# Kernel optimization log

Hardware: AMD Instinct MI355X
Metric: run time of the kernel (lower is better)

The kernel has to match this reference:

```python
import jax, jax.numpy as jnp
import numpy as np
import math

D_MODEL = 1024
N_HEADS = 16


def setup_inputs() -> dict:
    key = jax.random.key(0)
    ks = jax.random.split(key, 11)
    N, L, S = 2, 2048, 2048
    d = D_MODEL
    s = 1.0 / math.sqrt(d)
    return {
        "queries": jax.random.normal(ks[0], (N, L, d), dtype=jnp.float32),
        "keys": jax.random.normal(ks[1], (N, S, d), dtype=jnp.float32),
        "values": jax.random.normal(ks[2], (N, S, d), dtype=jnp.float32),
        # torch nn.Linear weights are [out_features, in_features]
        "Wq": jax.random.normal(ks[3], (d, d), dtype=jnp.float32) * s,
        "bq": jax.random.normal(ks[4], (d,), dtype=jnp.float32) * s,
        "Wk": jax.random.normal(ks[5], (d, d), dtype=jnp.float32) * s,
        "bk": jax.random.normal(ks[6], (d,), dtype=jnp.float32) * s,
        "Wv": jax.random.normal(ks[7], (d, d), dtype=jnp.float32) * s,
        "bv": jax.random.normal(ks[8], (d,), dtype=jnp.float32) * s,
        "Wo": jax.random.normal(ks[9], (d, d), dtype=jnp.float32) * s,
        "bo": jax.random.normal(ks[10], (d,), dtype=jnp.float32) * s,
    }


def reference(queries, keys, values, Wq, bq, Wk, bk, Wv, bv, Wo, bo):
    N, L, _ = queries.shape
    S = keys.shape[1]
    H = N_HEADS
    # projections (torch Linear: x @ W.T + b), reshape to heads
    q = (queries @ Wq.T + bq).reshape(N, L, H, -1)
    k = (keys @ Wk.T + bk).reshape(N, S, H, -1)
    v = (values @ Wv.T + bv).reshape(N, S, H, -1)
    D = k.shape[-1]
    # full attention score map [N, L, H, S]
    sm = jnp.einsum('nlhd,nshd->nlhs', q, k) / math.sqrt(D)
    # causal mask: position l attends to s <= l
    causal_mask = jnp.triu(jnp.ones((L, S), dtype=bool), k=1)  # True = masked
    sm = jnp.where(causal_mask[None, :, None, :], -jnp.inf, sm)
    sm = jax.nn.softmax(sm, axis=-1)
    attn = jnp.einsum('nlhs,nshd->nlhd', sm, v)  # [N, L, H, D]
    new_values = attn.reshape(N, L, H * D)
    return new_values @ Wo.T + bo
```

## Files before the change

kernel.cpp:

```cpp
#include <hip/hip_runtime.h>

typedef unsigned short u16;
typedef unsigned int u32;
typedef __attribute__((ext_vector_type(8))) short bf16x8;
typedef __attribute__((ext_vector_type(4))) float f32x4;
typedef __attribute__((ext_vector_type(16))) float f32x16;
typedef __attribute__((ext_vector_type(4))) float floatx4;
typedef __attribute__((ext_vector_type(4))) u16 u16x4;

__device__ __forceinline__ u16 f2bf(float x) {
  union { float f; u32 u; } c; c.f = x;
  return (u16)((c.u + 0x7fffu + ((c.u >> 16) & 1u)) >> 16);
}
__device__ __forceinline__ u32 packbf(float a, float b) {
  return (u32)f2bf(a) | ((u32)f2bf(b) << 16);
}
__device__ __forceinline__ u32 cvtpk(float lo, float hi) {
  u32 r;
  asm("v_cvt_pk_bf16_f32 %0, %1, %2" : "=v"(r) : "v"(lo), "v"(hi));
  return r;
}
__device__ __forceinline__ float bf2f(u16 v) {
  union { u32 u; float f; } c; c.u = (u32)v << 16; return c.f;
}

__device__ __forceinline__ void gload16(const u16* g, u16* l) {
  auto gp = (const __attribute__((address_space(1))) unsigned int*)g;
  auto lp = (__attribute__((address_space(3))) unsigned int*)l;
  __builtin_amdgcn_global_load_lds(gp, lp, 16, 0, 0);
}

__global__ void cvt7(const float* s0, const float* s1, const float* s2,
                     const float* s3, const float* s4, const float* s5, const float* s6,
                     u16* d0, u16* d1, u16* d2, u16* d3, u16* d4, u16* d5, u16* d6) {
  const int y = blockIdx.y;
  const float* s = (y == 0) ? s0 : (y == 1) ? s1 : (y == 2) ? s2 : (y == 3) ? s3
                  : (y == 4) ? s4 : (y == 5) ? s5 : s6;
  u16* d = (y == 0) ? d0 : (y == 1) ? d1 : (y == 2) ? d2 : (y == 3) ? d3
          : (y == 4) ? d4 : (y == 5) ? d5 : d6;
  const int n4 = (y < 3) ? (1 << 20) : (1 << 18);
  int i = blockIdx.x * 256 + threadIdx.x;
  if (i < n4) {
    floatx4 v = ((const floatx4*)s)[i];
    u16x4 o;
    o.x = f2bf(v.x); o.y = f2bf(v.y); o.z = f2bf(v.z); o.w = f2bf(v.w);
    ((u16x4*)d)[i] = o;
  }
}

__global__ __launch_bounds__(256) void gemm3(const u16* A0, const u16* A1, const u16* A2,
                                             const u16* W0, const u16* W1, const u16* W2,
                                             const float* b0, const float* b1, const float* b2,
                                             u16* o0, u16* o1, u16* o2) {
  __shared__ u16 lA[128 * 32];
  __shared__ u16 lB[128 * 32];
  const int z = blockIdx.z;
  const u16* A  = (z == 0) ? A0 : (z == 1) ? A1 : A2;
  const u16* Bw = (z == 0) ? W0 : (z == 1) ? W1 : W2;
  const float* bias = (z == 0) ? b0 : (z == 1) ? b1 : b2;
  u16* outp = (z == 0) ? o0 : (z == 1) ? o1 : o2;
  const float scl = (z == 0) ? (0.125f * 1.44269504089f) : 1.0f;

  const int tid = threadIdx.x;
  const int brow = blockIdx.y * 128, bcol = blockIdx.x * 128;
  const int lane = tid & 63, w = tid >> 6;
  const int wr = w >> 1, wc = w & 1;
  const int fr = lane & 15, fq = lane >> 4;
  f32x4 acc[4][4] = {};

  for (int k0 = 0; k0 < 1024; k0 += 32) {
    __syncthreads();
#pragma unroll
    for (int it = 0; it < 2; ++it) {
      int chunk = tid + it * 256;
      int row = chunk >> 2;
      int col = (chunk & 3) * 8;
      gload16(A  + (size_t)(brow + row) * 1024 + k0 + col, &lA[chunk * 8]);
      gload16(Bw + (size_t)(bcol + row) * 1024 + k0 + col, &lB[chunk * 8]);
    }
    __syncthreads();
    bf16x8 af[4], bfr[4];
#pragma unroll
    for (int m = 0; m < 4; ++m) af[m]  = *(const bf16x8*)&lA[(wr * 64 + m * 16 + fr) * 32 + fq * 8];
#pragma unroll
    for (int n = 0; n < 4; ++n) bfr[n] = *(const bf16x8*)&lB[(wc * 64 + n * 16 + fr) * 32 + fq * 8];
#pragma unroll
    for (int m = 0; m < 4; ++m)
#pragma unroll
      for (int n = 0; n < 4; ++n)
        acc[m][n] = __builtin_amdgcn_mfma_f32_16x16x32_bf16(af[m], bfr[n], acc[m][n], 0, 0, 0);
  }

#pragma unroll
  for (int m = 0; m < 4; ++m) {
#pragma unroll
    for (int n = 0; n < 4; ++n) {
      int colg = bcol + wc * 64 + n * 16 + fr;
      float bv = bias[colg];
#pragma unroll
      for (int j = 0; j < 4; ++j) {
        int rowg = brow + wr * 64 + m * 16 + fq * 4 + j;
        float v = (acc[m][n][j] + bv) * scl;
        int nb = rowg >> 11, l = rowg & 2047;
        int h = colg >> 6, dd = colg & 63;
        size_t idx = (z < 2) ? (((size_t)(nb * 16 + h) * 2048 + l) * 64 + dd)
                             : (((size_t)(nb * 16 + h) * 64 + dd) * 2048 + l);
        outp[idx] = f2bf(v);
      }
    }
  }
}

__global__ __launch_bounds__(256) void gemm_o(const u16* __restrict__ A,
                                              const u16* __restrict__ Bw,
                                              const float* __restrict__ bias,
                                              float* __restrict__ outp) {
  __shared__ u16 lA[128 * 32];
  __shared__ u16 lB[128 * 32];
  const int tid = threadIdx.x;
  const int brow = blockIdx.y * 128, bcol = blockIdx.x * 128;
  const int lane = tid & 63, w = tid >> 6;
  const int wr = w >> 1, wc = w & 1;
  const int fr = lane & 15, fq = lane >> 4;
  f32x4 acc[4][4] = {};

  for (int k0 = 0; k0 < 1024; k0 += 32) {
    __syncthreads();
#pragma unroll
    for (int it = 0; it < 2; ++it) {
      int chunk = tid + it * 256;
      int row = chunk >> 2;
      int col = (chunk & 3) * 8;
      gload16(A  + (size_t)(brow + row) * 1024 + k0 + col, &lA[chunk * 8]);
      gload16(Bw + (size_t)(bcol + row) * 1024 + k0 + col, &lB[chunk * 8]);
    }
    __syncthreads();
    bf16x8 af[4], bfr[4];
#pragma unroll
    for (int m = 0; m < 4; ++m) af[m]  = *(const bf16x8*)&lA[(wr * 64 + m * 16 + fr) * 32 + fq * 8];
#pragma unroll
    for (int n = 0; n < 4; ++n) bfr[n] = *(const bf16x8*)&lB[(wc * 64 + n * 16 + fr) * 32 + fq * 8];
#pragma unroll
    for (int m = 0; m < 4; ++m)
#pragma unroll
      for (int n = 0; n < 4; ++n)
        acc[m][n] = __builtin_amdgcn_mfma_f32_16x16x32_bf16(af[m], bfr[n], acc[m][n], 0, 0, 0);
  }

#pragma unroll
  for (int m = 0; m < 4; ++m) {
#pragma unroll
    for (int n = 0; n < 4; ++n) {
      int colg = bcol + wc * 64 + n * 16 + fr;
      float bv = bias[colg];
#pragma unroll
      for (int j = 0; j < 4; ++j) {
        int rowg = brow + wr * 64 + m * 16 + fq * 4 + j;
        outp[(size_t)rowg * 1024 + colg] = acc[m][n][j] + bv;
      }
    }
  }
}

__global__ __launch_bounds__(256) void attn_part(const u16* __restrict__ Qp,
                                                 const u16* __restrict__ Kp,
                                                 const u16* __restrict__ Vt,
                                                 u16* __restrict__ accP,
                                                 float* __restrict__ mP,
                                                 float* __restrict__ lP) {
  __shared__ u16 lK[2][2048];
  __shared__ u16 lV[2][2048];
  const int tid = threadIdx.x;
  const int lane = tid & 63, w = tid >> 6;
  const int bid = blockIdx.x;
  const int nh = bid / 40;
  const int j = bid - nh * 40;
  int p, t;
  if (j < 16)      { p = 0; t = j; }
  else if (j < 28) { p = 1; t = 4 + (j - 16); }
  else if (j < 36) { p = 2; t = 8 + (j - 28); }
  else             { p = 3; t = 12 + (j - 36); }
  const int i0 = p * 16;
  const int i1 = min(i0 + 16, (t + 1) * 4);
  const int col = lane & 31, hi = lane >> 5;
  const u16* Q = Qp + (size_t)nh * 2048 * 64;
  const u16* K = Kp + (size_t)nh * 2048 * 64;
  const u16* V = Vt + (size_t)nh * 64 * 2048;
  const int q = t * 128 + w * 32 + col;
  const int swz = (col & 7) << 4;

  const int kr  = tid >> 3;
  const int kin = ((tid & 7) * 16) ^ ((kr & 7) << 4);
  const int vd  = kr + ((kin >> 6) << 5);
  const int vs  = (kin & 63) >> 1;

  bf16x8 qf[4];
#pragma unroll
  for (int ks = 0; ks < 4; ++ks) qf[ks] = *(const bf16x8*)&Q[(size_t)q * 64 + ks * 16 + hi * 8];

  f32x16 acc0 = {}, acc1 = {};
  float mrow = -1e30f, lrow = 0.f;

  {
    const int s0 = i0 * 32;
    gload16(K + (size_t)(s0 + kr) * 64 + (kin >> 1), &lK[0][tid * 8]);
    gload16(V + (size_t)vd * 2048 + (s0 + vs),       &lV[0][tid * 8]);
  }
  __syncthreads();

  int cur = 0;
  for (int i = i0; i < i1; ++i) {
    if (i + 1 < i1) {
      const int s0n = (i + 1) * 32;
      gload16(K + (size_t)(s0n + kr) * 64 + (kin >> 1), &lK[cur ^ 1][tid * 8]);
      gload16(V + (size_t)vd * 2048 + (s0n + vs),       &lV[cur ^ 1][tid * 8]);
    }
    const int s0 = i * 32;
    f32x16 sc = {};
    __builtin_amdgcn_s_setprio(1);
#pragma unroll
    for (int ks = 0; ks < 4; ++ks) {
      bf16x8 kf = *(const bf16x8*)&lK[cur][col * 64 + (((ks * 32 + hi * 16) ^ swz) >> 1)];
      sc = __builtin_amdgcn_mfma_f32_32x32x16_bf16(kf, qf[ks], sc, 0, 0, 0);
    }
    __builtin_amdgcn_s_setprio(0);
    float pr[16];
    float pmax = -1e30f;
#pragma unroll
    for (int r = 0; r < 16; ++r) {
      int sr = (r & 3) + 8 * (r >> 2) + 4 * hi;
      float v = (s0 + sr > q) ? -1e30f : sc[r];
      pr[r] = v;
      pmax = fmaxf(pmax, v);
    }
    pmax = fmaxf(pmax, __shfl_xor(pmax, 32));
    if (!__all(pmax <= mrow + 8.f)) {
      float mnew = fmaxf(mrow, pmax);
      float alpha = exp2f(mrow - mnew);
#pragma unroll
      for (int r = 0; r < 16; ++r) { acc0[r] *= alpha; acc1[r] *= alpha; }
      lrow *= alpha;
      mrow = mnew;
    }
    float ps = 0.f;
#pragma unroll
    for (int r = 0; r < 16; ++r) { float pv = exp2f(pr[r] - mrow); pr[r] = pv; ps += pv; }
    ps += __shfl_xor(ps, 32);
    lrow += ps;

#pragma unroll
    for (int ks = 0; ks < 2; ++ks) {
      u32 A0 = cvtpk(pr[8 * ks + 0], pr[8 * ks + 1]);
      u32 A1 = cvtpk(pr[8 * ks + 2], pr[8 * ks + 3]);
      u32 B0 = cvtpk(pr[8 * ks + 4], pr[8 * ks + 5]);
      u32 B1 = cvtpk(pr[8 * ks + 6], pr[8 * ks + 7]);
      u32 t0 = __shfl_xor(hi ? A0 : B0, 32);
      u32 t1 = __shfl_xor(hi ? A1 : B1, 32);
      union { u32 u[4]; bf16x8 v; } pf;
      pf.u[0] = hi ? t0 : A0;
      pf.u[1] = hi ? t1 : A1;
      pf.u[2] = hi ? B0 : t0;
      pf.u[3] = hi ? B1 : t1;
      bf16x8 vf0 = *(const bf16x8*)&lV[cur][col * 64 + (((ks * 32 + hi * 16) ^ swz) >> 1)];
      bf16x8 vf1 = *(const bf16x8*)&lV[cur][col * 64 + (((64 + ks * 32 + hi * 16) ^ swz) >> 1)];
      __builtin_amdgcn_s_setprio(1);
      acc0 = __builtin_amdgcn_mfma_f32_32x32x16_bf16(vf0, pf.v, acc0, 0, 0, 0);
      acc1 = __builtin_amdgcn_mfma_f32_32x32x16_bf16(vf1, pf.v, acc1, 0, 0, 0);
      __builtin_amdgcn_s_setprio(0);
    }
    __syncthreads();
    cur ^= 1;
  }

  const int ql = w * 32 + col;
  u16* base = accP + (size_t)bid * 8192 + ql * 64;
#pragma unroll
  for (int rp = 0; rp < 8; ++rp) {
    int r = rp * 2;
    int d = (r & 3) + 8 * (r >> 2) + 4 * hi;
    *(u32*)&base[d]      = packbf(acc0[r], acc0[r + 1]);
    *(u32*)&base[32 + d] = packbf(acc1[r], acc1[r + 1]);
  }
  if (hi == 0) {
    mP[bid * 128 + ql] = mrow;
    lP[bid * 128 + ql] = lrow;
  }
}

__global__ void combineN(const u16* __restrict__ accP, const float* __restrict__ mP,
                         const float* __restrict__ lP, u16* __restrict__ at) {
  const int t = blockIdx.x >> 2;
  const int seg = blockIdx.x & 3;
  const int nh = blockIdx.y;
  const int ql = seg * 32 + (threadIdx.x >> 3);
  const int d0 = (threadIdx.x & 7) * 8;
  const int np = (t >> 2) + 1;
  const int s0 = nh * 40 + t;
  const int s1 = nh * 40 + 16 + (t - 4);
  const int s2 = nh * 40 + 28 + (t - 8);
  const int s3 = nh * 40 + 36 + (t - 12);

  float m = mP[s0 * 128 + ql];
  if (np > 1) m = fmaxf(m, mP[s1 * 128 + ql]);
  if (np > 2) m = fmaxf(m, mP[s2 * 128 + ql]);
  if (np > 3) m = fmaxf(m, mP[s3 * 128 + ql]);
  float w0 = exp2f(mP[s0 * 128 + ql] - m);
  float w1 = (np > 1) ? exp2f(mP[s1 * 128 + ql] - m) : 0.f;
  float w2 = (np > 2) ? exp2f(mP[s2 * 128 + ql] - m) : 0.f;
  float w3 = (np > 3) ? exp2f(mP[s3 * 128 + ql] - m) : 0.f;
  float l = lP[s0 * 128 + ql] * w0;
  if (np > 1) l += lP[s1 * 128 + ql] * w1;
  if (np > 2) l += lP[s2 * 128 + ql] * w2;
  if (np > 3) l += lP[s3 * 128 + ql] * w3;
  const float inv = 1.f / l;
  w0 *= inv; w1 *= inv; w2 *= inv; w3 *= inv;

  float o[8] = {};
  {
    const bf16x8 a = *(const bf16x8*)&accP[(size_t)s0 * 8192 + ql * 64 + d0];
#pragma unroll
    for (int k = 0; k < 8; ++k) o[k] += bf2f((u16)a[k]) * w0;
  }
  if (np > 1) {
    const bf16x8 a = *(const bf16x8*)&accP[(size_t)s1 * 8192 + ql * 64 + d0];
#pragma unroll
    for (int k = 0; k < 8; ++k) o[k] += bf2f((u16)a[k]) * w1;
  }
  if (np > 2) {
    const bf16x8 a = *(const bf16x8*)&accP[(size_t)s2 * 8192 + ql * 64 + d0];
#pragma unroll
    for (int k = 0; k < 8; ++k) o[k] += bf2f((u16)a[k]) * w2;
  }
  if (np > 3) {
    const bf16x8 a = *(const bf16x8*)&accP[(size_t)s3 * 8192 + ql * 64 + d0];
#pragma unroll
    for (int k = 0; k < 8; ++k) o[k] += bf2f((u16)a[k]) * w3;
  }

  const int nb = nh >> 4, h = nh & 15;
  u16* op = &at[((size_t)(nb * 2048 + t * 128 + ql)) * 1024 + h * 64 + d0];
#pragma unroll
  for (int jj = 0; jj < 4; ++jj)
    *(u32*)&op[2 * jj] = packbf(o[2 * jj], o[2 * jj + 1]);
}

extern "C" void kernel_launch(void* const* d_in, const int* in_sizes, int n_in,
                              void* d_out, int out_size, void* d_ws, size_t ws_size,
                              hipStream_t stream) {
  const float* queries = (const float*)d_in[0];
  const float* keys    = (const float*)d_in[1];
  const float* values  = (const float*)d_in[2];
  const float* Wq = (const float*)d_in[3]; const float* bq = (const float*)d_in[4];
  const float* Wk = (const float*)d_in[5]; const float* bk = (const float*)d_in[6];
  const float* Wv = (const float*)d_in[7]; const float* bv = (const float*)d_in[8];
  const float* Wo = (const float*)d_in[9]; const float* bo = (const float*)d_in[10];
  float* out = (float*)d_out;
  char* ws = (char*)d_ws;

  const size_t MB = 1u << 20;
  u16* xq  = (u16*)(ws + 0 * MB);
  u16* xk  = (u16*)(ws + 8 * MB);
  u16* xv  = (u16*)(ws + 16 * MB);
  u16* wqb = (u16*)(ws + 24 * MB);
  u16* wkb = (u16*)(ws + 26 * MB);
  u16* wvb = (u16*)(ws + 28 * MB);
  u16* wob = (u16*)(ws + 30 * MB);
  u16* qp  = (u16*)(ws + 32 * MB);
  u16* kp  = (u16*)(ws + 40 * MB);
  u16* vt  = (u16*)(ws + 48 * MB);
  u16* at  = xq;
  u16*   accP = (u16*)(ws + 8 * MB);
  float* mPp  = (float*)(ws + 28 * MB);
  float* lPp  = (float*)(ws + 28 * MB + 1280 * 128 * sizeof(float));

  cvt7<<<dim3(4096, 7), 256, 0, stream>>>(queries, keys, values, Wq, Wk, Wv, Wo,
                                          xq, xk, xv, wqb, wkb, wvb, wob);
  gemm3<<<dim3(8, 32, 3), 256, 0, stream>>>(xq, xk, xv, wqb, wkb, wvb,
                                            bq, bk, bv, qp, kp, vt);
  attn_part<<<1280, 256, 0, stream>>>(qp, kp, vt, accP, mPp, lPp);
  combineN<<<dim3(64, 32), 256, 0, stream>>>(accP, mPp, lPp, at);
  gemm_o<<<dim3(8, 32), 256, 0, stream>>>(at, wob, bo, out);
}
```

Measured before the change: 249.7 us.

## Double-buffer GEMM tiles, widen attention KV tiles, skip masked sub-tiles, remap blocks

```diff
diff --git a/kernel.cpp b/kernel.cpp
--- a/kernel.cpp
+++ b/kernel.cpp
@@ -29,6 +29,10 @@
   auto lp = (__attribute__((address_space(3))) unsigned int*)l;
   __builtin_amdgcn_global_load_lds(gp, lp, 16, 0, 0);
 }
+
+#define WAIT_VM4() asm volatile("s_waitcnt vmcnt(4)" ::: "memory")
+#define WAIT_VM0() asm volatile("s_waitcnt vmcnt(0)" ::: "memory")
+#define WAIT_LGKM0() asm volatile("s_waitcnt lgkmcnt(0)" ::: "memory")
 
 __global__ void cvt7(const float* s0, const float* s1, const float* s2,
                      const float* s3, const float* s4, const float* s5, const float* s6,
@@ -52,8 +56,8 @@
                                              const u16* W0, const u16* W1, const u16* W2,
                                              const float* b0, const float* b1, const float* b2,
                                              u16* o0, u16* o1, u16* o2) {
-  __shared__ u16 lA[128 * 32];
-  __shared__ u16 lB[128 * 32];
+  __shared__ u16 lA[2][128 * 32];
+  __shared__ u16 lB[2][128 * 32];
   const int z = blockIdx.z;
   const u16* A  = (z == 0) ? A0 : (z == 1) ? A1 : A2;
   const u16* Bw = (z == 0) ? W0 : (z == 1) ? W1 : W2;
@@ -68,27 +72,47 @@
   const int fr = lane & 15, fq = lane >> 4;
   f32x4 acc[4][4] = {};
 
-  for (int k0 = 0; k0 < 1024; k0 += 32) {
-    __syncthreads();
+  auto stageg = [&](int ks, int bb) {
 #pragma unroll
     for (int it = 0; it < 2; ++it) {
       int chunk = tid + it * 256;
       int row = chunk >> 2;
-      int col = (chunk & 3) * 8;
-      gload16(A  + (size_t)(brow + row) * 1024 + k0 + col, &lA[chunk * 8]);
-      gload16(Bw + (size_t)(bcol + row) * 1024 + k0 + col, &lB[chunk * 8]);
-    }
-    __syncthreads();
+      int colb = (chunk & 3) * 8;
+      gload16(A  + (size_t)(brow + row) * 1024 + ks * 32 + colb, &lA[bb][chunk * 8]);
+      gload16(Bw + (size_t)(bcol + row) * 1024 + ks * 32 + colb, &lB[bb][chunk * 8]);
+    }
+  };
+
+  float bvr[4];
+#pragma unroll
+  for (int n = 0; n < 4; ++n) bvr[n] = bias[bcol + wc * 64 + n * 16 + fr];
+
+  stageg(0, 0);
+  WAIT_VM0();
+  __builtin_amdgcn_s_barrier();
+
+  for (int kk = 0; kk < 32; ++kk) {
+    const int cur = kk & 1;
+    if (kk + 1 < 32) { stageg(kk + 1, cur ^ 1); WAIT_VM4(); }
+    else             { WAIT_VM0(); }
+    __builtin_amdgcn_s_barrier();
+    __builtin_amdgcn_sched_barrier(0);
+
     bf16x8 af[4], bfr[4];
 #pragma unroll
-    for (int m = 0; m < 4; ++m) af[m]  = *(const bf16x8*)&lA[(wr * 64 + m * 16 + fr) * 32 + fq * 8];
-#pragma unroll
-    for (int n = 0; n < 4; ++n) bfr[n] = *(const bf16x8*)&lB[(wc * 64 + n * 16 + fr) * 32 + fq * 8];
+    for (int m = 0; m < 4; ++m) af[m]  = *(const bf16x8*)&lA[cur][(wr * 64 + m * 16 + fr) * 32 + fq * 8];
+#pragma unroll
+    for (int n = 0; n < 4; ++n) bfr[n] = *(const bf16x8*)&lB[cur][(wc * 64 + n * 16 + fr) * 32 + fq * 8];
+    __builtin_amdgcn_s_setprio(1);
 #pragma unroll
     for (int m = 0; m < 4; ++m)
 #pragma unroll
       for (int n = 0; n < 4; ++n)
         acc[m][n] = __builtin_amdgcn_mfma_f32_16x16x32_bf16(af[m], bfr[n], acc[m][n], 0, 0, 0);
+    __builtin_amdgcn_s_setprio(0);
+
+    WAIT_LGKM0();
+    __builtin_amdgcn_s_barrier();
   }
 
 #pragma unroll
@@ -96,11 +120,10 @@
 #pragma unroll
     for (int n = 0; n < 4; ++n) {
       int colg = bcol + wc * 64 + n * 16 + fr;
-      float bv = bias[colg];
 #pragma unroll
       for (int j = 0; j < 4; ++j) {
         int rowg = brow + wr * 64 + m * 16 + fq * 4 + j;
-        float v = (acc[m][n][j] + bv) * scl;
+        float v = (acc[m][n][j] + bvr[n]) * scl;
         int nb = rowg >> 11, l = rowg & 2047;
         int h = colg >> 6, dd = colg & 63;
         size_t idx = (z < 2) ? (((size_t)(nb * 16 + h) * 2048 + l) * 64 + dd)
@@ -115,8 +138,8 @@
                                               const u16* __restrict__ Bw,
                                               const float* __restrict__ bias,
                                               float* __restrict__ outp) {
-  __shared__ u16 lA[128 * 32];
-  __shared__ u16 lB[128 * 32];
+  __shared__ u16 lA[2][128 * 32];
+  __shared__ u16 lB[2][128 * 32];
   const int tid = threadIdx.x;
   const int brow = blockIdx.y * 128, bcol = blockIdx.x * 128;
   const int lane = tid & 63, w = tid >> 6;
@@ -124,27 +147,47 @@
   const int fr = lane & 15, fq = lane >> 4;
   f32x4 acc[4][4] = {};
 
-  for (int k0 = 0; k0 < 1024; k0 += 32) {
-    __syncthreads();
+  auto stageg = [&](int ks, int bb) {
 #pragma unroll
     for (int it = 0; it < 2; ++it) {
       int chunk = tid + it * 256;
       int row = chunk >> 2;
-      int col = (chunk & 3) * 8;
-      gload16(A  + (size_t)(brow + row) * 1024 + k0 + col, &lA[chunk * 8]);
-      gload16(Bw + (size_t)(bcol + row) * 1024 + k0 + col, &lB[chunk * 8]);
-    }
-    __syncthreads();
+      int colb = (chunk & 3) * 8;
+      gload16(A  + (size_t)(brow + row) * 1024 + ks * 32 + colb, &lA[bb][chunk * 8]);
+      gload16(Bw + (size_t)(bcol + row) * 1024 + ks * 32 + colb, &lB[bb][chunk * 8]);
+    }
+  };
+
+  float bvr[4];
+#pragma unroll
+  for (int n = 0; n < 4; ++n) bvr[n] = bias[bcol + wc * 64 + n * 16 + fr];
+
+  stageg(0, 0);
+  WAIT_VM0();
+  __builtin_amdgcn_s_barrier();
+
+  for (int kk = 0; kk < 32; ++kk) {
+    const int cur = kk & 1;
+    if (kk + 1 < 32) { stageg(kk + 1, cur ^ 1); WAIT_VM4(); }
+    else             { WAIT_VM0(); }
+    __builtin_amdgcn_s_barrier();
+    __builtin_amdgcn_sched_barrier(0);
+
     bf16x8 af[4], bfr[4];
 #pragma unroll
-    for (int m = 0; m < 4; ++m) af[m]  = *(const bf16x8*)&lA[(wr * 64 + m * 16 + fr) * 32 + fq * 8];
-#pragma unroll
-    for (int n = 0; n < 4; ++n) bfr[n] = *(const bf16x8*)&lB[(wc * 64 + n * 16 + fr) * 32 + fq * 8];
+    for (int m = 0; m < 4; ++m) af[m]  = *(const bf16x8*)&lA[cur][(wr * 64 + m * 16 + fr) * 32 + fq * 8];
+#pragma unroll
+    for (int n = 0; n < 4; ++n) bfr[n] = *(const bf16x8*)&lB[cur][(wc * 64 + n * 16 + fr) * 32 + fq * 8];
+    __builtin_amdgcn_s_setprio(1);
 #pragma unroll
     for (int m = 0; m < 4; ++m)
 #pragma unroll
       for (int n = 0; n < 4; ++n)
         acc[m][n] = __builtin_amdgcn_mfma_f32_16x16x32_bf16(af[m], bfr[n], acc[m][n], 0, 0, 0);
+    __builtin_amdgcn_s_setprio(0);
+
+    WAIT_LGKM0();
+    __builtin_amdgcn_s_barrier();
   }
 
 #pragma unroll
@@ -152,11 +195,10 @@
 #pragma unroll
     for (int n = 0; n < 4; ++n) {
       int colg = bcol + wc * 64 + n * 16 + fr;
-      float bv = bias[colg];
 #pragma unroll
       for (int j = 0; j < 4; ++j) {
         int rowg = brow + wr * 64 + m * 16 + fq * 4 + j;
-        outp[(size_t)rowg * 1024 + colg] = acc[m][n][j] + bv;
+        outp[(size_t)rowg * 1024 + colg] = acc[m][n][j] + bvr[n];
       }
     }
   }
@@ -168,112 +210,132 @@
                                                  u16* __restrict__ accP,
                                                  float* __restrict__ mP,
                                                  float* __restrict__ lP) {
-  __shared__ u16 lK[2][2048];
-  __shared__ u16 lV[2][2048];
+  __shared__ u16 lK[2][4096];
+  __shared__ u16 lV[2][4096];
   const int tid = threadIdx.x;
   const int lane = tid & 63, w = tid >> 6;
-  const int bid = blockIdx.x;
-  const int nh = bid / 40;
-  const int j = bid - nh * 40;
+  const int bid = (int)blockIdx.x;
+  const int vbid = (bid & 7) * 160 + (bid >> 3);
+  const int nh = vbid / 40;
+  const int j = vbid - nh * 40;
   int p, t;
   if (j < 16)      { p = 0; t = j; }
   else if (j < 28) { p = 1; t = 4 + (j - 16); }
   else if (j < 36) { p = 2; t = 8 + (j - 28); }
   else             { p = 3; t = 12 + (j - 36); }
-  const int i0 = p * 16;
-  const int i1 = min(i0 + 16, (t + 1) * 4);
+  const int P0 = p * 8;
+  const int P1 = min(P0 + 8, 2 * (t + 1));
   const int col = lane & 31, hi = lane >> 5;
   const u16* Q = Qp + (size_t)nh * 2048 * 64;
   const u16* K = Kp + (size_t)nh * 2048 * 64;
   const u16* V = Vt + (size_t)nh * 64 * 2048;
-  const int q = t * 128 + w * 32 + col;
+  const int qbase = t * 128 + w * 32;
+  const int q = qbase + col;
   const int swz = (col & 7) << 4;
 
-  const int kr  = tid >> 3;
-  const int kin = ((tid & 7) * 16) ^ ((kr & 7) << 4);
-  const int vd  = kr + ((kin >> 6) << 5);
-  const int vs  = (kin & 63) >> 1;
+  auto stage = [&](int pp, int bb) {
+#pragma unroll
+    for (int it = 0; it < 2; ++it) {
+      int c = tid + it * 256;
+      int kr = c >> 3;
+      int kin = ((c & 7) * 16) ^ ((kr & 7) << 4);
+      gload16(K + (size_t)(pp * 64 + kr) * 64 + (kin >> 1), &lK[bb][c * 8]);
+      int tt = c >> 8, cc = c & 255;
+      int lr = cc >> 3;
+      int vin = ((cc & 7) * 16) ^ ((lr & 7) << 4);
+      int vd = lr + ((vin >> 6) << 5);
+      gload16(V + (size_t)vd * 2048 + pp * 64 + tt * 32 + ((vin & 63) >> 1),
+              &lV[bb][c * 8]);
+    }
+  };
 
   bf16x8 qf[4];
 #pragma unroll
   for (int ks = 0; ks < 4; ++ks) qf[ks] = *(const bf16x8*)&Q[(size_t)q * 64 + ks * 16 + hi * 8];
 
   f32x16 acc0 = {}, acc1 = {};
-  float mrow = -1e30f, lrow = 0.f;
-
-  {
-    const int s0 = i0 * 32;
-    gload16(K + (size_t)(s0 + kr) * 64 + (kin >> 1), &lK[0][tid * 8]);
-    gload16(V + (size_t)vd * 2048 + (s0 + vs),       &lV[0][tid * 8]);
-  }
-  __syncthreads();
-
-  int cur = 0;
-  for (int i = i0; i < i1; ++i) {
-    if (i + 1 < i1) {
-      const int s0n = (i + 1) * 32;
-      gload16(K + (size_t)(s0n + kr) * 64 + (kin >> 1), &lK[cur ^ 1][tid * 8]);
-      gload16(V + (size_t)vd * 2048 + (s0n + vs),       &lV[cur ^ 1][tid * 8]);
-    }
-    const int s0 = i * 32;
-    f32x16 sc = {};
-    __builtin_amdgcn_s_setprio(1);
-#pragma unroll
-    for (int ks = 0; ks < 4; ++ks) {
-      bf16x8 kf = *(const bf16x8*)&lK[cur][col * 64 + (((ks * 32 + hi * 16) ^ swz) >> 1)];
-      sc = __builtin_amdgcn_mfma_f32_32x32x16_bf16(kf, qf[ks], sc, 0, 0, 0);
-    }
-    __builtin_amdgcn_s_setprio(0);
-    float pr[16];
-    float pmax = -1e30f;
-#pragma unroll
-    for (int r = 0; r < 16; ++r) {
-      int sr = (r & 3) + 8 * (r >> 2) + 4 * hi;
-      float v = (s0 + sr > q) ? -1e30f : sc[r];
-      pr[r] = v;
-      pmax = fmaxf(pmax, v);
-    }
-    pmax = fmaxf(pmax, __shfl_xor(pmax, 32));
-    if (!__all(pmax <= mrow + 8.f)) {
-      float mnew = fmaxf(mrow, pmax);
-      float alpha = exp2f(mrow - mnew);
-#pragma unroll
-      for (int r = 0; r < 16; ++r) { acc0[r] *= alpha; acc1[r] *= alpha; }
-      lrow *= alpha;
-      mrow = mnew;
-    }
-    float ps = 0.f;
-#pragma unroll
-    for (int r = 0; r < 16; ++r) { float pv = exp2f(pr[r] - mrow); pr[r] = pv; ps += pv; }
-    ps += __shfl_xor(ps, 32);
-    lrow += ps;
-
-#pragma unroll
-    for (int ks = 0; ks < 2; ++ks) {
-      u32 A0 = cvtpk(pr[8 * ks + 0], pr[8 * ks + 1]);
-      u32 A1 = cvtpk(pr[8 * ks + 2], pr[8 * ks + 3]);
-      u32 B0 = cvtpk(pr[8 * ks + 4], pr[8 * ks + 5]);
-      u32 B1 = cvtpk(pr[8 * ks + 6], pr[8 * ks + 7]);
-      u32 t0 = __shfl_xor(hi ? A0 : B0, 32);
-      u32 t1 = __shfl_xor(hi ? A1 : B1, 32);
-      union { u32 u[4]; bf16x8 v; } pf;
-      pf.u[0] = hi ? t0 : A0;
-      pf.u[1] = hi ? t1 : A1;
-      pf.u[2] = hi ? B0 : t0;
-      pf.u[3] = hi ? B1 : t1;
-      bf16x8 vf0 = *(const bf16x8*)&lV[cur][col * 64 + (((ks * 32 + hi * 16) ^ swz) >> 1)];
-      bf16x8 vf1 = *(const bf16x8*)&lV[cur][col * 64 + (((64 + ks * 32 + hi * 16) ^ swz) >> 1)];
+  float mrow = -1e30f, lsum = 0.f;
+
+  stage(P0, 0);
+  WAIT_VM0();
+  __builtin_amdgcn_s_barrier();
+
+  for (int pp = P0; pp < P1; ++pp) {
+    const int buf = (pp - P0) & 1;
+    if (pp + 1 < P1) { stage(pp + 1, buf ^ 1); WAIT_VM4(); }
+    else             { WAIT_VM0(); }
+    __builtin_amdgcn_s_barrier();
+    __builtin_amdgcn_sched_barrier(0);
+
+#pragma unroll
+    for (int tt = 0; tt < 2; ++tt) {
+      const int s0 = pp * 64 + tt * 32;
+      if (s0 > qbase) continue;
+      f32x16 sc = {};
       __builtin_amdgcn_s_setprio(1);
-      acc0 = __builtin_amdgcn_mfma_f32_32x32x16_bf16(vf0, pf.v, acc0, 0, 0, 0);
-      acc1 = __builtin_amdgcn_mfma_f32_32x32x16_bf16(vf1, pf.v, acc1, 0, 0, 0);
+#pragma unroll
+      for (int ks = 0; ks < 4; ++ks) {
+        bf16x8 kf = *(const bf16x8*)&lK[buf][(tt * 32 + col) * 64 + (((ks * 32 + hi * 16) ^ swz) >> 1)];
+        sc = __builtin_amdgcn_mfma_f32_32x32x16_bf16(kf, qf[ks], sc, 0, 0, 0);
+      }
       __builtin_amdgcn_s_setprio(0);
-    }
-    __syncthreads();
-    cur ^= 1;
+      float pr[16];
+      float pmax = -1e30f;
+      if (s0 == qbase) {
+#pragma unroll
+        for (int r = 0; r < 16; ++r) {
+          int sr = (r & 3) + 8 * (r >> 2) + 4 * hi;
+          float v = (sr > col) ? -1e30f : sc[r];
+          pr[r] = v;
+          pmax = fmaxf(pmax, v);
+        }
+      } else {
+#pragma unroll
+        for (int r = 0; r < 16; ++r) { pr[r] = sc[r]; pmax = fmaxf(pmax, sc[r]); }
+      }
+      pmax = fmaxf(pmax, __shfl_xor(pmax, 32));
+      if (!__all(pmax <= mrow + 8.f)) {
+        float mnew = fmaxf(mrow, pmax);
+        float alpha = exp2f(mrow - mnew);
+#pragma unroll
+        for (int r = 0; r < 16; ++r) { acc0[r] *= alpha; acc1[r] *= alpha; }
+        lsum *= alpha;
+        mrow = mnew;
+      }
+      float ps = 0.f;
+#pragma unroll
+      for (int r = 0; r < 16; ++r) { float pv = exp2f(pr[r] - mrow); pr[r] = pv; ps += pv; }
+      ps += __shfl_xor(ps, 32);
+      lsum += ps;
+
+#pragma unroll
+      for (int ks = 0; ks < 2; ++ks) {
+        u32 A0 = cvtpk(pr[8 * ks + 0], pr[8 * ks + 1]);
+        u32 A1 = cvtpk(pr[8 * ks + 2], pr[8 * ks + 3]);
+        u32 B0 = cvtpk(pr[8 * ks + 4], pr[8 * ks + 5]);
+        u32 B1 = cvtpk(pr[8 * ks + 6], pr[8 * ks + 7]);
+        u32 t0 = __shfl_xor(hi ? A0 : B0, 32);
+        u32 t1 = __shfl_xor(hi ? A1 : B1, 32);
+        union { u32 u[4]; bf16x8 v; } pf;
+        pf.u[0] = hi ? t0 : A0;
+        pf.u[1] = hi ? t1 : A1;
+        pf.u[2] = hi ? B0 : t0;
+        pf.u[3] = hi ? B1 : t1;
+        bf16x8 vf0 = *(const bf16x8*)&lV[buf][tt * 2048 + col * 64 + (((ks * 32 + hi * 16) ^ swz) >> 1)];
+        bf16x8 vf1 = *(const bf16x8*)&lV[buf][tt * 2048 + col * 64 + (((64 + ks * 32 + hi * 16) ^ swz) >> 1)];
+        __builtin_amdgcn_s_setprio(1);
+        acc0 = __builtin_amdgcn_mfma_f32_32x32x16_bf16(vf0, pf.v, acc0, 0, 0, 0);
+        acc1 = __builtin_amdgcn_mfma_f32_32x32x16_bf16(vf1, pf.v, acc1, 0, 0, 0);
+        __builtin_amdgcn_s_setprio(0);
+      }
+    }
+
+    WAIT_LGKM0();
+    __builtin_amdgcn_s_barrier();
   }
 
   const int ql = w * 32 + col;
-  u16* base = accP + (size_t)bid * 8192 + ql * 64;
+  u16* base = accP + (size_t)vbid * 8192 + ql * 64;
 #pragma unroll
   for (int rp = 0; rp < 8; ++rp) {
     int r = rp * 2;
@@ -282,8 +344,8 @@
     *(u32*)&base[32 + d] = packbf(acc1[r], acc1[r + 1]);
   }
   if (hi == 0) {
-    mP[bid * 128 + ql] = mrow;
-    lP[bid * 128 + ql] = lrow;
+    mP[vbid * 128 + ql] = mrow;
+    lP[vbid * 128 + ql] = lsum;
   }
 }
 
```

New measurement: 245.7 us. About the same (-1.6%).
